# Performance work log

Hardware: AMD Instinct MI355X
Metric: run time of the kernel (lower is better)

## Reference

```python
import jax, jax.numpy as jnp
import numpy as np
from jax import lax

# STE sign: forward maps x>=0 -> +1, x<0 -> -1 (matches XORQuantizeSTE)
@jax.custom_vjp
def ste_sign(x):
    return jnp.where(x >= 0, jnp.ones_like(x), -jnp.ones_like(x))

def _ste_fwd(x):
    return ste_sign(x), None

def _ste_bwd(_, g):
    return (g,)  # identity pass-through

ste_sign.defvjp(_ste_fwd, _ste_bwd)


def _xor_quant(x, w):
    """Per-layer XNOR-Net quantization: alpha = mean|W| scales both
    binarized activation and binarized weight (as in the wrapper's hook
    + binarization())."""
    alpha = jnp.mean(jnp.abs(w))
    return alpha * ste_sign(x), alpha * ste_sign(w)


def _conv(x, w, b, stride):
    y = lax.conv_general_dilated(
        x, w, window_strides=(stride, stride), padding=((1, 1), (1, 1)),
        dimension_numbers=('NCHW', 'OIHW', 'NCHW'))
    return y + b[None, :, None, None]


def setup_inputs() -> dict:
    key = jax.random.key(0)
    ks = jax.random.split(key, 9)
    f32 = jnp.float32
    x = jax.random.normal(ks[0], (32, 3, 224, 224), dtype=f32)
    w1 = jax.random.normal(ks[1], (64, 3, 3, 3), dtype=f32) * 0.1
    b1 = jax.random.normal(ks[2], (64,), dtype=f32) * 0.01
    w2 = jax.random.normal(ks[3], (128, 64, 3, 3), dtype=f32) * 0.05
    b2 = jax.random.normal(ks[4], (128,), dtype=f32) * 0.01
    w3 = jax.random.normal(ks[5], (256, 128, 3, 3), dtype=f32) * 0.03
    b3 = jax.random.normal(ks[6], (256,), dtype=f32) * 0.01
    wf = jax.random.normal(ks[7], (1000, 256), dtype=f32) * 0.05
    bf = jax.random.normal(ks[8], (1000,), dtype=f32) * 0.01
    return {'x': x, 'w1': w1, 'b1': b1, 'w2': w2, 'b2': b2,
            'w3': w3, 'b3': b3, 'wf': wf, 'bf': bf}


def reference(x, w1, b1, w2, b2, w3, b3, wf, bf):
    # layer 1: binarize activation + weight with shared alpha, dense conv
    xq, wq = _xor_quant(x, w1)
    h = jnp.clip(_conv(xq, wq, b1, 2), -1.0, 1.0)   # [32,64,112,112]
    xq, wq = _xor_quant(h, w2)
    h = jnp.clip(_conv(xq, wq, b2, 2), -1.0, 1.0)   # [32,128,56,56]
    xq, wq = _xor_quant(h, w3)
    h = jnp.clip(_conv(xq, wq, b3, 2), -1.0, 1.0)   # [32,256,28,28]
    h = jnp.mean(h, axis=(2, 3))                     # global avg pool [32,256]
    xq, wq = _xor_quant(h, wf)
    return xq @ wq.T + bf                            # [32,1000]
```

## Files before the change

### kernel.cpp

```cpp
#include <hip/hip_runtime.h>
#include <stdint.h>
#include <math.h>


#define A_OFF      0ull
#define WP2_OFF    2048ull
#define WP3T_OFF   16384ull
#define WFP_OFF    65536ull
#define PART_OFF   100352ull
#define P1_OFF     102400ull
#define P2_OFF     3313664ull
#define POOLP_OFF  4919296ull

__global__ __launch_bounds__(256) void k1_conv1_pack(
    const float* __restrict__ x,  const float* __restrict__ w1, const float* __restrict__ b1,
    const float* __restrict__ w2, const float* __restrict__ w3, const float* __restrict__ wf,
    uint64_t* __restrict__ wp2, uint64_t* __restrict__ wp3t, uint64_t* __restrict__ wfp,
    double* __restrict__ part, uint64_t* __restrict__ p1)
{
    const int tid = threadIdx.x, lane = tid & 63, bid = blockIdx.x;
    if (bid < 1568) {
        __shared__ double sd[256];
        __shared__ uint32_t wm[64];
        double s = 0.0;
        for (int i = tid; i < 1728; i += 256) s += fabs((double)w1[i]);
        sd[tid] = s;
        if (tid < 64) {
            uint32_t m = 0;
            for (int t = 0; t < 27; t++) {
                int ci = t / 9, r = t % 9, kh = r / 3, kw = r % 3;
                if (w1[((tid*3 + ci)*3 + kh)*3 + kw] >= 0.f) m |= (1u << t);
            }
            wm[tid] = m;
        }
        __syncthreads();
        for (int off = 128; off > 0; off >>= 1) {
            if (tid < off) sd[tid] += sd[tid + off];
            __syncthreads();
        }
        double a = sd[0] / 1728.0;
        double a2 = a * a;

        int idx = bid * 256 + tid;
        int wo = idx % 112, t1 = idx / 112;
        int ho = t1 % 112, n = t1 / 112;
        uint32_t xm = 0, vm = 0;
        #pragma unroll
        for (int ci = 0; ci < 3; ci++)
            #pragma unroll
            for (int kh = 0; kh < 3; kh++) {
                int hi = 2*ho + kh - 1;
                if ((unsigned)hi >= 224u) continue;
                #pragma unroll
                for (int kw = 0; kw < 3; kw++) {
                    int wi = 2*wo + kw - 1;
                    if ((unsigned)wi >= 224u) continue;
                    int t = ci*9 + kh*3 + kw;
                    vm |= (1u << t);
                    if (x[((n*3 + ci)*224 + hi)*224 + wi] >= 0.f) xm |= (1u << t);
                }
            }
        int V = __popc(vm);
        uint64_t bits = 0;
        for (int co = 0; co < 64; co++) {
            int m = __popc((~(xm ^ wm[co])) & vm);
            double h = a2 * (double)(2*m - V) + (double)b1[co];
            if (h >= 0.0) bits |= (1ull << co);
        }
        p1[idx] = bits;
    } else {
        int rel = bid - 1568;
        if (rel < 96) {
            __shared__ double sd[256];
            int t = rel >> 5, c = rel & 31;
            const float* w; int n;
            if (t == 0)      { w = w2; n = 128*64*9; }
            else if (t == 1) { w = w3; n = 256*128*9; }
            else             { w = wf; n = 1000*256; }
            int per = (n + 31) / 32;
            int lo = c * per, hi = min(n, lo + per);
            double s0 = 0.0, s1 = 0.0, s2 = 0.0, s3 = 0.0;
            int i = lo + tid;
            for (; i + 768 < hi; i += 1024) {
                s0 += fabs((double)w[i]);
                s1 += fabs((double)w[i + 256]);
                s2 += fabs((double)w[i + 512]);
                s3 += fabs((double)w[i + 768]);
            }
            for (; i < hi; i += 256) s0 += fabs((double)w[i]);
            sd[tid] = (s0 + s1) + (s2 + s3);
            __syncthreads();
            for (int off = 128; off > 0; off >>= 1) {
                if (tid < off) sd[tid] += sd[tid + off];
                __syncthreads();
            }
            if (tid == 0) part[(t + 1)*32 + c] = sd[0];
        }
        int gw = rel * 4 + (tid >> 6);
        const int nw = 640;
        for (int w = gw; w < 1152; w += nw) {
            int co = w / 9, tap = w % 9, kh = tap / 3, kw = tap % 3;
            uint64_t b = __ballot(w2[((co*64 + lane)*3 + kh)*3 + kw] >= 0.f);
            if (lane == 0) wp2[w] = b;
        }
        for (int w = gw; w < 4608; w += nw) {
            int co = w / 18, r = w % 18, tap = r / 2, half = r & 1;
            int kh = tap / 3, kw = tap % 3;
            uint64_t b = __ballot(w3[((co*128 + half*64 + lane)*3 + kh)*3 + kw] >= 0.f);
            if (lane == 0) wp3t[(tap*2 + half)*256 + co] = b;
        }
        for (int w = gw; w < 4000; w += nw) {
            int o = w >> 2, j = w & 3;
            uint64_t b = __ballot(wf[o*256 + j*64 + lane] >= 0.f);
            if (lane == 0) wfp[w] = b;
        }
    }
}

__global__ __launch_bounds__(256) void k2_conv2(
    const uint64_t* __restrict__ p1, const float* __restrict__ b2,
    const double* __restrict__ part, const uint64_t* __restrict__ wp2g,
    uint32_t* __restrict__ p2)
{
    __shared__ uint64_t wp[1152];
    const int tid = threadIdx.x, lane = tid & 63;
    for (int i = tid; i < 1152; i += 256) wp[i] = wp2g[i];
    double s = 0.0;
    for (int j = 0; j < 32; j++) s += part[32 + j];
    double a = s / (double)(128*64*9);
    double a2 = a * a;
    __syncthreads();
    int q = tid >> 6;
    int co0 = q * 32;
    int pos = blockIdx.x * 64 + lane;
    int wo = pos % 56, t1 = pos / 56;
    int ho = t1 % 56, n = t1 / 56;
    uint64_t xv[9]; uint64_t vmask[9]; int V = 0;
    #pragma unroll
    for (int kh = 0; kh < 3; kh++)
        #pragma unroll
        for (int kw = 0; kw < 3; kw++) {
            int t = kh*3 + kw;
            int hi = 2*ho + kh - 1, wi = 2*wo + kw - 1;
            bool ok = ((unsigned)hi < 112u) && ((unsigned)wi < 112u);
            vmask[t] = ok ? ~0ull : 0ull;
            xv[t] = ok ? p1[(n*112 + hi)*112 + wi] : 0ull;
            V += ok ? 1 : 0;
        }
    int base = 64 * V;
    uint32_t bits = 0;
    for (int c = 0; c < 32; c++) {
        int co = co0 + c;
        int m = 0;
        #pragma unroll
        for (int t = 0; t < 9; t++)
            m += __popcll((xv[t] ^ wp[co*9 + t]) & vmask[t]);
        double h = a2 * (double)(base - 2*m) + (double)b2[co];
        if (h >= 0.0) bits |= (1u << c);
    }
    p2[pos*4 + q] = bits;
}

__global__ __launch_bounds__(256) void k3_conv3pool(
    const uint64_t* __restrict__ p2, const float* __restrict__ b3,
    const double* __restrict__ part, const uint64_t* __restrict__ wp3t,
    double* __restrict__ partial)
{
    __shared__ uint64_t xs[28*18];
    const int tid = threadIdx.x;
    int n = blockIdx.x / 28, ho = blockIdx.x % 28;

    double s = 0.0;
    for (int j = 0; j < 32; j++) s += part[64 + j];
    double a = s / (double)(256*128*9);
    double a2 = a * a;

    uint64_t w[18];
    #pragma unroll
    for (int i = 0; i < 18; i++) w[i] = wp3t[i*256 + tid];
    uint32_t P[9];
    #pragma unroll
    for (int t = 0; t < 9; t++) P[t] = __popcll(w[2*t]) + __popcll(w[2*t+1]);

    for (int i = tid; i < 504; i += 256) {
        int wo = i / 18, r = i % 18;
        int tap = r / 2, half = r % 2;
        int kh = tap / 3, kw = tap % 3;
        int hi = 2*ho + kh - 1, wi = 2*wo + kw - 1;
        bool ok = ((unsigned)hi < 56u) && ((unsigned)wi < 56u);
        xs[i] = ok ? p2[(size_t)((n*56 + hi)*56 + wi)*2 + half] : 0ull;
    }
    __syncthreads();

    bool htop = (ho == 0);
    int rv = htop ? 2 : 3;
    double bc = (double)b3[tid];
    double sum = 0.0;
    for (int wo = 0; wo < 28; wo++) {
        int mm = 0;
        #pragma unroll
        for (int t = 0; t < 18; t++)
            mm += __popcll(xs[wo*18 + t] ^ w[t]);
        bool wl = (wo == 0);
        int cv = wl ? 2 : 3;
        int corr = 0;
        if (htop) corr += P[0] + P[1] + P[2];
        if (wl)   corr += P[0] + P[3] + P[6];
        if (htop && wl) corr -= P[0];
        int dot = 128*(rv*cv) - 2*mm + 2*corr;
        double h = a2 * (double)dot + bc;
        h = fmin(fmax(h, -1.0), 1.0);
        sum += h;
    }
    partial[(size_t)(n*28 + ho)*256 + tid] = sum;
}

__global__ __launch_bounds__(256) void k4_poolfc(
    const double* __restrict__ partial, const uint64_t* __restrict__ wfp,
    const float* __restrict__ bf, const double* __restrict__ part,
    float* __restrict__ out)
{
    __shared__ uint64_t spl[4];
    const int tid = threadIdx.x, lane = tid & 63;
    int n = blockIdx.x;
    double s = 0.0;
    for (int c = 0; c < 28; c++) s += partial[(size_t)(n*28 + c)*256 + tid];
    uint64_t bal = __ballot((s / 784.0) >= 0.0);
    if (lane == 0) spl[tid >> 6] = bal;

    double sa = 0.0;
    for (int j = 0; j < 32; j++) sa += part[96 + j];
    double a = sa / (double)(1000*256);
    double aa = a * a;
    __syncthreads();
    uint64_t s0 = spl[0], s1 = spl[1], s2 = spl[2], s3 = spl[3];
    for (int o = tid; o < 1000; o += 256) {
        int m = __popcll(s0 ^ wfp[o*4]) + __popcll(s1 ^ wfp[o*4+1])
              + __popcll(s2 ^ wfp[o*4+2]) + __popcll(s3 ^ wfp[o*4+3]);
        out[n*1000 + o] = (float)(aa * (double)(256 - 2*m) + (double)bf[o]);
    }
}

extern "C" void kernel_launch(void* const* d_in, const int* in_sizes, int n_in,
                              void* d_out, int out_size, void* d_ws, size_t ws_size,
                              hipStream_t stream) {
    const float* x  = (const float*)d_in[0];
    const float* w1 = (const float*)d_in[1];
    const float* b1 = (const float*)d_in[2];
    const float* w2 = (const float*)d_in[3];
    const float* b2 = (const float*)d_in[4];
    const float* w3 = (const float*)d_in[5];
    const float* b3 = (const float*)d_in[6];
    const float* wf = (const float*)d_in[7];
    const float* bf = (const float*)d_in[8];

    char* ws = (char*)d_ws;
    uint64_t* wp2    = (uint64_t*)(ws + WP2_OFF);
    uint64_t* wp3t   = (uint64_t*)(ws + WP3T_OFF);
    uint64_t* wfp    = (uint64_t*)(ws + WFP_OFF);
    double*   part   = (double*)  (ws + PART_OFF);
    uint64_t* p1     = (uint64_t*)(ws + P1_OFF);
    uint32_t* p2     = (uint32_t*)(ws + P2_OFF);
    double*   poolp  = (double*)  (ws + POOLP_OFF);
    float*    out    = (float*)   d_out;

    hipLaunchKernelGGL(k1_conv1_pack, dim3(1728), dim3(256), 0, stream,
                       x, w1, b1, w2, w3, wf, wp2, wp3t, wfp, part, p1);
    hipLaunchKernelGGL(k2_conv2,      dim3(1568), dim3(256), 0, stream,
                       p1, b2, part, wp2, p2);
    hipLaunchKernelGGL(k3_conv3pool,  dim3(896),  dim3(256), 0, stream,
                       (const uint64_t*)p2, b3, part, wp3t, poolp);
    hipLaunchKernelGGL(k4_poolfc,     dim3(32),   dim3(256), 0, stream,
                       poolp, wfp, bf, part, out);
}
```

Measured before the change: 151.0 us.

## Precompute border-correction table for conv2 and stage inputs/bias in shared memory

In conv2, padded taps are zeroed in the activation tile so the per-tap valid masks can be dropped from the inner popcount loop. A per-channel correction table indexed by border configuration (top/left) restores the exact dot product. Activations for the block are loaded once into shared memory instead of each of the four waves reloading them, and biases are cached as doubles. In conv1, the alpha reduction moves from a block-wide shared-memory tree to a single-wave shuffle reduction, so one barrier replaces nine. The extra setup and barrier in conv2 are the cost of these changes.

```diff
diff --git a/kernel.cpp b/kernel.cpp
--- a/kernel.cpp
+++ b/kernel.cpp
@@ -3,7 +3,6 @@
 #include <math.h>
 
 
-#define A_OFF      0ull
 #define WP2_OFF    2048ull
 #define WP3T_OFF   16384ull
 #define WFP_OFF    65536ull
@@ -18,29 +17,28 @@
     uint64_t* __restrict__ wp2, uint64_t* __restrict__ wp3t, uint64_t* __restrict__ wfp,
     double* __restrict__ part, uint64_t* __restrict__ p1)
 {
-    const int tid = threadIdx.x, lane = tid & 63, bid = blockIdx.x;
+    const int tid = threadIdx.x, lane = tid & 63, wid = tid >> 6, bid = blockIdx.x;
     if (bid < 1568) {
-        __shared__ double sd[256];
+        __shared__ double a2s;
+        __shared__ double db1[64];
         __shared__ uint32_t wm[64];
-        double s = 0.0;
-        for (int i = tid; i < 1728; i += 256) s += fabs((double)w1[i]);
-        sd[tid] = s;
-        if (tid < 64) {
+        if (wid == 0) {
+            double s = 0.0;
+            #pragma unroll
+            for (int i = 0; i < 27; i++) s += fabs((double)w1[lane + i*64]);
+            #pragma unroll
+            for (int off = 1; off < 64; off <<= 1) s += __shfl_xor(s, off, 64);
+            if (lane == 0) { double a = s / 1728.0; a2s = a * a; }
+        } else if (wid == 1) {
             uint32_t m = 0;
             for (int t = 0; t < 27; t++) {
                 int ci = t / 9, r = t % 9, kh = r / 3, kw = r % 3;
-                if (w1[((tid*3 + ci)*3 + kh)*3 + kw] >= 0.f) m |= (1u << t);
+                if (w1[((lane*3 + ci)*3 + kh)*3 + kw] >= 0.f) m |= (1u << t);
             }
-            wm[tid] = m;
-        }
-        __syncthreads();
-        for (int off = 128; off > 0; off >>= 1) {
-            if (tid < off) sd[tid] += sd[tid + off];
-            __syncthreads();
-        }
-        double a = sd[0] / 1728.0;
-        double a2 = a * a;
-
+            wm[lane] = m;
+        } else if (wid == 2) {
+            db1[lane] = (double)b1[lane];
+        }
         int idx = bid * 256 + tid;
         int wo = idx % 112, t1 = idx / 112;
         int ho = t1 % 112, n = t1 / 112;
@@ -60,11 +58,13 @@
                     if (x[((n*3 + ci)*224 + hi)*224 + wi] >= 0.f) xm |= (1u << t);
                 }
             }
+        __syncthreads();
+        double a2 = a2s;
         int V = __popc(vm);
         uint64_t bits = 0;
         for (int co = 0; co < 64; co++) {
             int m = __popc((~(xm ^ wm[co])) & vm);
-            double h = a2 * (double)(2*m - V) + (double)b1[co];
+            double h = a2 * (double)(2*m - V) + db1[co];
             if (h >= 0.0) bits |= (1ull << co);
         }
         p1[idx] = bits;
@@ -96,7 +96,7 @@
             }
             if (tid == 0) part[(t + 1)*32 + c] = sd[0];
         }
-        int gw = rel * 4 + (tid >> 6);
+        int gw = rel * 4 + wid;
         const int nw = 640;
         for (int w = gw; w < 1152; w += nw) {
             int co = w / 9, tap = w % 9, kh = tap / 3, kw = tap % 3;
@@ -123,39 +123,64 @@
     uint32_t* __restrict__ p2)
 {
     __shared__ uint64_t wp[1152];
+    __shared__ uint64_t xs[9*64];
+    __shared__ int      dtab[128*4];
+    __shared__ double   db2[128];
     const int tid = threadIdx.x, lane = tid & 63;
+
     for (int i = tid; i < 1152; i += 256) wp[i] = wp2g[i];
+    if (tid < 128) db2[tid] = (double)b2[tid];
+    for (int i = tid; i < 576; i += 256) {
+        int t = i / 64, pl = i % 64;
+        int pos = blockIdx.x * 64 + pl;
+        int wo = pos % 56, t1 = pos / 56;
+        int ho = t1 % 56, n = t1 / 56;
+        int kh = t / 3, kw = t % 3;
+        int hi = 2*ho + kh - 1, wi = 2*wo + kw - 1;
+        bool ok = ((unsigned)hi < 112u) && ((unsigned)wi < 112u);
+        xs[t*64 + pl] = ok ? p1[(n*112 + hi)*112 + wi] : 0ull;
+    }
     double s = 0.0;
     for (int j = 0; j < 32; j++) s += part[32 + j];
     double a = s / (double)(128*64*9);
     double a2 = a * a;
     __syncthreads();
+    if (tid < 128) {
+        int co = tid;
+        uint32_t P[9];
+        #pragma unroll
+        for (int t = 0; t < 9; t++) P[t] = __popcll(wp[co*9 + t]);
+        int cT = P[0] + P[1] + P[2];
+        int cL = P[0] + P[3] + P[6];
+        int cC = P[0];
+        #pragma unroll
+        for (int cfg = 0; cfg < 4; cfg++) {
+            int isT = cfg & 1, isL = (cfg >> 1) & 1;
+            int V = 9 - 3*isT - 3*isL + (isT & isL);
+            int corr = isT*cT + isL*cL - (isT & isL)*cC;
+            dtab[co*4 + cfg] = 64*V + 2*corr;
+        }
+    }
+    __syncthreads();
+
     int q = tid >> 6;
     int co0 = q * 32;
     int pos = blockIdx.x * 64 + lane;
     int wo = pos % 56, t1 = pos / 56;
-    int ho = t1 % 56, n = t1 / 56;
-    uint64_t xv[9]; uint64_t vmask[9]; int V = 0;
+    int ho = t1 % 56;
+    int cfg = (ho == 0 ? 1 : 0) | (wo == 0 ? 2 : 0);
+    uint64_t xv[9];
     #pragma unroll
-    for (int kh = 0; kh < 3; kh++)
-        #pragma unroll
-        for (int kw = 0; kw < 3; kw++) {
-            int t = kh*3 + kw;
-            int hi = 2*ho + kh - 1, wi = 2*wo + kw - 1;
-            bool ok = ((unsigned)hi < 112u) && ((unsigned)wi < 112u);
-            vmask[t] = ok ? ~0ull : 0ull;
-            xv[t] = ok ? p1[(n*112 + hi)*112 + wi] : 0ull;
-            V += ok ? 1 : 0;
-        }
-    int base = 64 * V;
+    for (int t = 0; t < 9; t++) xv[t] = xs[t*64 + lane];
     uint32_t bits = 0;
     for (int c = 0; c < 32; c++) {
         int co = co0 + c;
-        int m = 0;
+        int mm = 0;
         #pragma unroll
         for (int t = 0; t < 9; t++)
-            m += __popcll((xv[t] ^ wp[co*9 + t]) & vmask[t]);
-        double h = a2 * (double)(base - 2*m) + (double)b2[co];
+            mm += __popcll(xv[t] ^ wp[co*9 + t]);
+        int dot = dtab[co*4 + cfg] - 2*mm;
+        double h = a2 * (double)dot + db2[co];
         if (h >= 0.0) bits |= (1u << c);
     }
     p2[pos*4 + q] = bits;
```

Measured after the change: 146.1 us. 1.03x faster.
